# Kernel tuning notes

Measured on AMD Instinct MI355X. Metric: run time of the kernel, lower is better.

The kernel has to match this reference:

```python
import jax, jax.numpy as jnp
import numpy as np

N = 50000        # n_nodes
E = 640000       # n_edges
D = 128          # d_model (in_dim == out_dim)
H = 8            # num_heads
DH = D // H      # head dim = 16
EPS = 1e-5


def _batchnorm(x, g, b):
    # BatchNorm1d, training-mode batch statistics (biased variance)
    mu = jnp.mean(x, axis=0)
    var = jnp.mean((x - mu) ** 2, axis=0)
    return (x - mu) * jax.lax.rsqrt(var + EPS) * g + b


def setup_inputs() -> dict:
    key = jax.random.key(0)
    ks = jax.random.split(key, 16)
    s = 0.05
    h = jax.random.normal(ks[0], (N, D), jnp.float32)
    src = jax.random.randint(ks[1], (E,), 0, N)
    # guarantee every node has >= 1 incoming edge (avoids z == 0)
    dst = jnp.concatenate([jnp.arange(N), jax.random.randint(ks[2], (E - N,), 0, N)])
    return {
        "h": h,
        "src": src,
        "dst": dst,
        "WQ": jax.random.normal(ks[3], (D, D), jnp.float32) * s,
        "WK": jax.random.normal(ks[4], (D, D), jnp.float32) * s,
        "WV": jax.random.normal(ks[5], (D, D), jnp.float32) * s,
        "WO": jax.random.normal(ks[6], (D, D), jnp.float32) * s,
        "bO": jnp.zeros((D,), jnp.float32),
        "W1": jax.random.normal(ks[7], (2 * D, D), jnp.float32) * s,
        "b1": jnp.zeros((2 * D,), jnp.float32),
        "W2": jax.random.normal(ks[8], (D, 2 * D), jnp.float32) * s,
        "b2": jnp.zeros((D,), jnp.float32),
        "bn1_g": jnp.ones((D,), jnp.float32),
        "bn1_b": jnp.zeros((D,), jnp.float32),
        "bn2_g": jnp.ones((D,), jnp.float32),
        "bn2_b": jnp.zeros((D,), jnp.float32),
    }


def reference(h, src, dst, WQ, WK, WV, WO, bO, W1, b1, W2, b2, bn1_g, bn1_b, bn2_g, bn2_b):
    n = h.shape[0]
    # projections -> [N, H, DH]
    Q = (h @ WQ.T).reshape(n, H, DH)
    K = (h @ WK.T).reshape(n, H, DH)
    V = (h @ WV.T).reshape(n, H, DH)
    # per-edge score: sum(K[src] * Q[dst]) -> [E, H]; clamp/exp (scaled_exp)
    score = jnp.sum(K[src] * Q[dst], axis=-1) / np.sqrt(DH)
    score = jnp.exp(jnp.clip(score, -5.0, 5.0))
    # scatter-sum weighted values and normalizers to destination nodes
    wV = jax.ops.segment_sum(V[src] * score[..., None], dst, num_segments=n)  # [N,H,DH]
    z = jax.ops.segment_sum(score, dst, num_segments=n)                       # [N,H]
    attn = (wV / z[..., None]).reshape(n, D)
    # O projection + residual + BN1
    h1 = _batchnorm(h + (attn @ WO.T + bO), bn1_g, bn1_b)
    # FFN + residual + BN2
    f = jax.nn.relu(h1 @ W1.T + b1) @ W2.T + b2
    return _batchnorm(h1 + f, bn2_g, bn2_b)
```

## Files before the change

kernel.cpp:

```cpp
#include <hip/hip_runtime.h>
#include <math.h>


#define ND128 16384
typedef _Float16 f16;
typedef __attribute__((ext_vector_type(8))) _Float16 h8;
typedef __attribute__((ext_vector_type(4))) _Float16 h4;
typedef __attribute__((ext_vector_type(2))) _Float16 h2;
typedef __attribute__((ext_vector_type(4))) float f4;
typedef __attribute__((ext_vector_type(2))) float ff2;

__device__ __forceinline__ float fast_exp2(float x) {
#if __has_builtin(__builtin_amdgcn_exp2f)
    return __builtin_amdgcn_exp2f(x);
#else
    return exp2f(x);
#endif
}

template <int CTRL>
__device__ __forceinline__ float dppadd(float x) {
    int t = __builtin_amdgcn_update_dpp(0, __float_as_int(x), CTRL, 0xF, 0xF, false);
    return x + __int_as_float(t);
}
__device__ __forceinline__ float wsum8(float p) {
    p = dppadd<0xB1>(p);
    p = dppadd<0x4E>(p);
    p = dppadd<0x141>(p);
    return p;
}

__device__ __forceinline__ ff2 fp8x2_dec_sw(unsigned v) {
    ff2 r;
    unsigned b0 = v & 0xffu, b1 = (v >> 8) & 0xffu;
    {
        unsigned e = (b0 >> 3) & 15u, m = b0 & 7u;
        float x = e ? __uint_as_float(((e + 120u) << 23) | (m << 20)) : (float)m * 0.001953125f;
        r.x = (b0 & 0x80u) ? -x : x;
    }
    {
        unsigned e = (b1 >> 3) & 15u, m = b1 & 7u;
        float x = e ? __uint_as_float(((e + 120u) << 23) | (m << 20)) : (float)m * 0.001953125f;
        r.y = (b1 & 0x80u) ? -x : x;
    }
    return r;
}

__device__ __forceinline__ ff2 dec_lo(unsigned v) {
#if __has_builtin(__builtin_amdgcn_cvt_pk_f32_fp8)
    return __builtin_amdgcn_cvt_pk_f32_fp8((int)v, false);
#else
    return fp8x2_dec_sw(v & 0xffffu);
#endif
}
__device__ __forceinline__ ff2 dec_hi(unsigned v) {
#if __has_builtin(__builtin_amdgcn_cvt_pk_f32_fp8)
    return __builtin_amdgcn_cvt_pk_f32_fp8((int)v, true);
#else
    return fp8x2_dec_sw((v >> 16) & 0xffffu);
#endif
}

#if !__has_builtin(__builtin_amdgcn_cvt_pk_fp8_f32)
__device__ __forceinline__ unsigned char fp8_1(float f) {
    float a = fabsf(f);
    unsigned sg = (__float_as_uint(f) >> 31) << 7;
    if (a >= 448.f) return (unsigned char)(sg | 0x7E);
    if (a < 0.0009765625f) return (unsigned char)sg;
    int E; float m = frexpf(a, &E);
    if (E - 1 < -6) {
        int q = (int)rintf(a * 512.f);
        if (q > 7) return (unsigned char)(sg | 0x08);
        return (unsigned char)(sg | q);
    }
    int q = (int)rintf(m * 16.f);
    if (q == 16) { q = 8; E += 1; }
    int Ef = E - 1 + 7;
    if (Ef > 15) return (unsigned char)(sg | 0x7E);
    return (unsigned char)(sg | (Ef << 3) | (q - 8));
}
#endif

__device__ __forceinline__ unsigned short fp8_pack2(float a0, float a1) {
#if __has_builtin(__builtin_amdgcn_cvt_pk_fp8_f32)
    int pk = __builtin_amdgcn_cvt_pk_fp8_f32(a0, a1, 0, false);
    return (unsigned short)(pk & 0xffff);
#else
    return (unsigned short)((unsigned)fp8_1(a0) | ((unsigned)fp8_1(a1) << 8));
#endif
}

__global__ __launch_bounds__(256) void k_prep_hist(
    const float* __restrict__ WQ, const float* __restrict__ WK,
    const float* __restrict__ WV, const float* __restrict__ WO,
    const float* __restrict__ W2,
    f16* __restrict__ Wqb, f16* __restrict__ Wkb,
    f16* __restrict__ Wvb, f16* __restrict__ Wob, f16* __restrict__ W2b,
    int* __restrict__ cursor, const int* __restrict__ dst,
    int N, int E, int nhb)
{
    const int tid = threadIdx.x;
    if (blockIdx.x < (unsigned)nhb) {
        int e = blockIdx.x * 256 + tid;
        if (e < E) atomicAdd(&cursor[dst[e]], 1);
        return;
    }
    const int ws = blockIdx.x - nhb;
    const float* Wsrc; f16* dstw; int K, base;
    if (ws < 4) {
        Wsrc = ws == 0 ? WQ : ws == 1 ? WK : ws == 2 ? WV : WO;
        dstw = ws == 0 ? Wqb : ws == 1 ? Wkb : ws == 2 ? Wvb : Wob;
        K = 128; base = 0;
    } else {
        Wsrc = W2; dstw = W2b; K = 256; base = (ws - 4) * 2048;
    }
#pragma unroll
    for (int it = 0; it < 8; ++it) {
        int cid = base + it * 256 + tid;
        int lane = cid & 63;
        int kb, nt;
        if (K == 128) { kb = (cid >> 6) & 3; nt = cid >> 8; }
        else          { kb = (cid >> 6) & 7; nt = cid >> 9; }
        int row = nt * 16 + (lane & 15);
        int col = kb * 32 + (lane >> 4) * 8;
        const float* pp = Wsrc + (size_t)row * K + col;
        f16 o8[8];
#pragma unroll
        for (int j = 0; j < 8; ++j) o8[j] = (f16)pp[j];
        *(h8*)(dstw + (size_t)cid * 8) = *(const h8*)o8;
    }
}

__global__ __launch_bounds__(512) void k_qkvf(
    const float* __restrict__ h, f16* __restrict__ hb,
    const f16* __restrict__ Wqb, const f16* __restrict__ Wkb,
    const f16* __restrict__ Wvb,
    f16* __restrict__ Qb, unsigned char* __restrict__ KV8,
    const int* __restrict__ cursor, int* __restrict__ bsum, int N, int nsb)
{
    __shared__ f16 sA[ND128];
    __shared__ int ws8[8];
    const int tid = threadIdx.x;
    if (blockIdx.x < (unsigned)nsb) {
        int base = blockIdx.x * 2048 + tid * 4;
        int s = 0;
#pragma unroll
        for (int j = 0; j < 4; ++j) {
            int idx = base + j;
            if (idx < N) s += cursor[idx];
        }
#pragma unroll
        for (int off = 32; off; off >>= 1) s += __shfl_down(s, off, 64);
        if ((tid & 63) == 0) ws8[tid >> 6] = s;
        __syncthreads();
        if (tid == 0) {
            int r = 0;
#pragma unroll
            for (int k = 0; k < 8; ++k) r += ws8[k];
            bsum[blockIdx.x] = r;
        }
        return;
    }
    const int slab = blockIdx.x - nsb;
#pragma unroll
    for (int it = 0; it < 4; ++it) {
        int cid = it * 512 + tid;
        int lane = cid & 63;
        int m = (cid >> 6) & 7;
        int kb = cid >> 9;
        int row = slab * 128 + m * 16 + (lane & 15);
        int col = kb * 32 + (lane >> 4) * 8;
        f16 o8[8];
        if (row < N) {
            const float* pp = h + (size_t)row * 128 + col;
            float4 f0 = *(const float4*)pp;
            float4 f1 = *(const float4*)(pp + 4);
            o8[0] = (f16)f0.x; o8[1] = (f16)f0.y; o8[2] = (f16)f0.z; o8[3] = (f16)f0.w;
            o8[4] = (f16)f1.x; o8[5] = (f16)f1.y; o8[6] = (f16)f1.z; o8[7] = (f16)f1.w;
        } else {
#pragma unroll
            for (int j = 0; j < 8; ++j) o8[j] = (f16)0.f;
        }
        h8 v = *(const h8*)o8;
        *(h8*)(hb + (size_t)slab * ND128 + (size_t)cid * 8) = v;
        *(h8*)(sA + (size_t)cid * 8) = v;
    }
    __syncthreads();

    const int w2 = tid >> 6, lane = tid & 63;
    const int rl = lane & 15, quad = lane >> 4;
#pragma unroll
    for (int oidx = 0; oidx < 3; ++oidx) {
        const f16* __restrict__ Wb = oidx == 0 ? Wqb : oidx == 1 ? Wkb : Wvb;
        h8 bfr[4];
#pragma unroll
        for (int kb = 0; kb < 4; ++kb)
            bfr[kb] = *(const h8*)(Wb + (size_t)((w2 * 4 + kb) * 64 + lane) * 8);

        f4 acc[8];
        f4 zero = {0.f, 0.f, 0.f, 0.f};
#pragma unroll
        for (int m = 0; m < 8; ++m) acc[m] = zero;
#pragma unroll
        for (int m = 0; m < 8; ++m) {
#pragma unroll
            for (int kb = 0; kb < 4; ++kb) {
                h8 a = *(const h8*)(sA + (size_t)((kb * 8 + m) * 64 + lane) * 8);
                acc[m] = __builtin_amdgcn_mfma_f32_16x16x32_f16(bfr[kb], a, acc[m], 0, 0, 0);
            }
        }
        if (oidx == 0) {
#pragma unroll
            for (int m = 0; m < 8; ++m) {
                int gr = slab * 128 + m * 16 + rl;
                if (gr < N) {
                    h4 o;
                    o[0] = (f16)acc[m][0]; o[1] = (f16)acc[m][1];
                    o[2] = (f16)acc[m][2]; o[3] = (f16)acc[m][3];
                    *(h4*)(Qb + (size_t)gr * 128 + w2 * 16 + quad * 4) = o;
                }
            }
        } else {
            const int koff = (oidx == 2) ? 2 : 0;
#pragma unroll
            for (int m = 0; m < 8; ++m) {
                int gr = slab * 128 + m * 16 + rl;
                if (gr < N) {
                    int c0 = w2 * 16 + quad * 4;
                    unsigned short p01 = fp8_pack2(acc[m][0], acc[m][1]);
                    unsigned short p23 = fp8_pack2(acc[m][2], acc[m][3]);
                    unsigned char* rowp = KV8 + (size_t)gr * 256 + (size_t)c0 * 2 + koff;
                    *(unsigned short*)(rowp) = p01;
                    *(unsigned short*)(rowp + 4) = p23;
                }
            }
        }
    }
}

__global__ __launch_bounds__(256) void k_scanC(
    const int* __restrict__ cnt, const int* __restrict__ bsum,
    int* __restrict__ rowptr, int* __restrict__ cursor, int N, int nsb)
{
    const int t = threadIdx.x, b = blockIdx.x;
    __shared__ int sboff;
    if (t == 0) {
        int r = 0;
        for (int i2 = 0; i2 < b; ++i2) r += bsum[i2];
        sboff = r;
    }
    if (t == 64 && b == nsb - 1) {
        int r = 0;
        for (int i2 = 0; i2 < nsb; ++i2) r += bsum[i2];
        rowptr[N] = r;
    }
    int base = b * 2048 + t * 8;
    int loc[8];
    int s = 0;
#pragma unroll
    for (int j = 0; j < 8; ++j) {
        int idx = base + j;
        loc[j] = (idx < N) ? cnt[idx] : 0;
        s += loc[j];
    }
    __shared__ int part[256];
    part[t] = s;
    __syncthreads();
    for (int off = 1; off < 256; off <<= 1) {
        int v = (t >= off) ? part[t - off] : 0;
        __syncthreads();
        part[t] += v;
        __syncthreads();
    }
    int run = sboff + (t ? part[t - 1] : 0);
#pragma unroll
    for (int j = 0; j < 8; ++j) {
        int idx = base + j;
        if (idx < N) { rowptr[idx] = run; cursor[idx] = run; run += loc[j]; }
    }
}

__global__ __launch_bounds__(256) void k_scatter(
    const int* __restrict__ src, const int* __restrict__ dst,
    int* __restrict__ cursor, int* __restrict__ csr_src, int E)
{
    int e = blockIdx.x * 256 + threadIdx.x;
    if (e < E) {
        int pos = atomicAdd(&cursor[dst[e]], 1);
        csr_src[pos] = src[e];
    }
}

__global__ __launch_bounds__(256) void k_attn(
    const f16* __restrict__ Qb, const unsigned char* __restrict__ KV8,
    const int* __restrict__ rowptr, const int* __restrict__ csr_src,
    f16* __restrict__ attnf, int N)
{
    const int node = blockIdx.x * 4 + (threadIdx.x >> 6);
    const int lane = threadIdx.x & 63;
    if (node >= N) return;
    const int beg = rowptr[node], end = rowptr[node + 1];

    float qx, qy;
    {
        h2 q2 = ((const h2*)(Qb + (size_t)node * 128))[lane];
        const float SCL = 0.25f * 1.44269504f;
        qx = (float)q2[0] * SCL;
        qy = (float)q2[1] * SCL;
    }
    const float CLP = 5.f * 1.44269504f;
    const unsigned loff = 4u * (unsigned)lane;

    float axA = 0.f, ayA = 0.f, axB = 0.f, ayB = 0.f, zA = 0.f, zB = 0.f;
    int i = beg;
    for (; i + 7 < end; i += 8) {
        int s[8];
#pragma unroll
        for (int u = 0; u < 8; ++u) s[u] = csr_src[i + u];
        unsigned kv[8];
#pragma unroll
        for (int u = 0; u < 8; ++u)
            kv[u] = *(const unsigned*)(KV8 + (size_t)s[u] * 256 + loff);
        float p[8];
#pragma unroll
        for (int u = 0; u < 8; ++u) {
            ff2 kf = dec_lo(kv[u]);
            p[u] = fmaf(qx, kf.x, qy * kf.y);
        }
#pragma unroll
        for (int u = 0; u < 8; ++u) p[u] = wsum8(p[u]);
        float sc[8];
#pragma unroll
        for (int u = 0; u < 8; ++u)
            sc[u] = fast_exp2(fminf(fmaxf(p[u], -CLP), CLP));
#pragma unroll
        for (int u = 0; u < 8; ++u) {
            ff2 vf = dec_hi(kv[u]);
            if (u & 1) {
                axB = fmaf(vf.x, sc[u], axB); ayB = fmaf(vf.y, sc[u], ayB); zB += sc[u];
            } else {
                axA = fmaf(vf.x, sc[u], axA); ayA = fmaf(vf.y, sc[u], ayA); zA += sc[u];
            }
        }
    }
    if (i + 3 < end) {
        int s[4];
#pragma unroll
        for (int u = 0; u < 4; ++u) s[u] = csr_src[i + u];
        unsigned kv[4];
#pragma unroll
        for (int u = 0; u < 4; ++u)
            kv[u] = *(const unsigned*)(KV8 + (size_t)s[u] * 256 + loff);
#pragma unroll
        for (int u = 0; u < 4; ++u) {
            ff2 kf = dec_lo(kv[u]);
            float p = wsum8(fmaf(qx, kf.x, qy * kf.y));
            float scu = fast_exp2(fminf(fmaxf(p, -CLP), CLP));
            ff2 vf = dec_hi(kv[u]);
            if (u & 1) {
                axB = fmaf(vf.x, scu, axB); ayB = fmaf(vf.y, scu, ayB); zB += scu;
            } else {
                axA = fmaf(vf.x, scu, axA); ayA = fmaf(vf.y, scu, ayA); zA += scu;
            }
        }
        i += 4;
    }
    for (; i < end; ++i) {
        int s0 = csr_src[i];
        unsigned kv = *(const unsigned*)(KV8 + (size_t)s0 * 256 + loff);
        ff2 kf = dec_lo(kv);
        float p0 = wsum8(fmaf(qx, kf.x, qy * kf.y));
        float sc0 = fast_exp2(fminf(fmaxf(p0, -CLP), CLP));
        ff2 vf = dec_hi(kv);
        axA = fmaf(vf.x, sc0, axA); ayA = fmaf(vf.y, sc0, ayA);
        zA += sc0;
    }
    float inv = 1.f / (zA + zB);
    h2 o2;
    o2[0] = (f16)((axA + axB) * inv);
    o2[1] = (f16)((ayA + ayB) * inv);
    int slab = node >> 7, m = (node >> 4) & 7, lr = node & 15;
    int kb = lane >> 4, quad2 = (lane & 15) >> 2, j = (lane & 3) * 2;
    *(h2*)(attnf + (size_t)slab * ND128 +
           (size_t)(((kb * 8 + m) * 64 + lr + 16 * quad2) * 8 + j)) = o2;
}

__global__ __launch_bounds__(256) void k_oproj(
    const f16* __restrict__ attnf, const f16* __restrict__ Wob,
    const f16* __restrict__ hbf, const float* __restrict__ bO,
    f16* __restrict__ t1b, float* __restrict__ bn, int N)
{
    __shared__ float csum[128], csq[128];
    const int tid = threadIdx.x, slab = blockIdx.x;
    const int w = tid >> 6, lane = tid & 63;
    if (tid < 128) { csum[tid] = 0.f; csq[tid] = 0.f; }
    __syncthreads();
    const f16* A = attnf + (size_t)slab * ND128;
    const f16* HB = hbf + (size_t)slab * ND128;

    h8 bfr[2][4];
#pragma unroll
    for (int nt = 0; nt < 2; ++nt)
#pragma unroll
        for (int kb = 0; kb < 4; ++kb)
            bfr[nt][kb] = *(const h8*)(Wob + (size_t)(((2 * w + nt) * 4 + kb) * 64 + lane) * 8);

    f4 acc[8][2];
    f4 zero = {0.f, 0.f, 0.f, 0.f};
#pragma unroll
    for (int m = 0; m < 8; ++m) { acc[m][0] = zero; acc[m][1] = zero; }
#pragma unroll
    for (int m = 0; m < 8; ++m) {
#pragma unroll
        for (int kb = 0; kb < 4; ++kb) {
            h8 a = *(const h8*)(A + (size_t)((kb * 8 + m) * 64 + lane) * 8);
            acc[m][0] = __builtin_amdgcn_mfma_f32_16x16x32_f16(bfr[0][kb], a, acc[m][0], 0, 0, 0);
            acc[m][1] = __builtin_amdgcn_mfma_f32_16x16x32_f16(bfr[1][kb], a, acc[m][1], 0, 0, 0);
        }
    }

    const int rl = lane & 15, quad = lane >> 4;
    float4 bo[2];
#pragma unroll
    for (int nt = 0; nt < 2; ++nt)
        bo[nt] = *(const float4*)(bO + w * 32 + nt * 16 + quad * 4);
    float pcs[2][4], pcq[2][4];
#pragma unroll
    for (int nt = 0; nt < 2; ++nt)
#pragma unroll
        for (int r = 0; r < 4; ++r) { pcs[nt][r] = 0.f; pcq[nt][r] = 0.f; }

#pragma unroll
    for (int m = 0; m < 8; ++m) {
        int gr = slab * 128 + m * 16 + rl;
        if (gr < N) {
#pragma unroll
            for (int nt = 0; nt < 2; ++nt) {
                size_t fidx = (size_t)(((w * 8 + m) * 64 + (nt * 2 + (quad >> 1)) * 16 + rl) * 8 +
                                       (quad & 1) * 4);
                h4 hv4 = *(const h4*)(HB + fidx);
                float v0 = acc[m][nt][0] + (float)hv4[0] + bo[nt].x;
                float v1 = acc[m][nt][1] + (float)hv4[1] + bo[nt].y;
                float v2 = acc[m][nt][2] + (float)hv4[2] + bo[nt].z;
                float v3 = acc[m][nt][3] + (float)hv4[3] + bo[nt].w;
                h4 o; o[0] = (f16)v0; o[1] = (f16)v1; o[2] = (f16)v2; o[3] = (f16)v3;
                *(h4*)(t1b + (size_t)slab * ND128 + fidx) = o;
                pcs[nt][0] += v0; pcq[nt][0] += v0 * v0;
                pcs[nt][1] += v1; pcq[nt][1] += v1 * v1;
                pcs[nt][2] += v2; pcq[nt][2] += v2 * v2;
                pcs[nt][3] += v3; pcq[nt][3] += v3 * v3;
            }
        }
    }
#pragma unroll
    for (int nt = 0; nt < 2; ++nt)
#pragma unroll
        for (int r = 0; r < 4; ++r) {
            float s = pcs[nt][r], q = pcq[nt][r];
            s += __shfl_xor(s, 8, 16); q += __shfl_xor(q, 8, 16);
            s += __shfl_xor(s, 4, 16); q += __shfl_xor(q, 4, 16);
            s += __shfl_xor(s, 2, 16); q += __shfl_xor(q, 2, 16);
            s += __shfl_xor(s, 1, 16); q += __shfl_xor(q, 1, 16);
            if (rl == 0) {
                int cl = w * 32 + nt * 16 + quad * 4 + r;
                atomicAdd(&csum[cl], s);
                atomicAdd(&csq[cl], q);
            }
        }
    __syncthreads();
    if (tid < 128) {
        atomicAdd(bn + tid, csum[tid]);
        atomicAdd(bn + 128 + tid, csq[tid]);
    }
}

__global__ __launch_bounds__(128) void k_fold1(
    const float* __restrict__ bn, const float* __restrict__ g1,
    const float* __restrict__ bb1, const float* __restrict__ W1,
    const float* __restrict__ b1, f16* __restrict__ W1b,
    float* __restrict__ badj, float* __restrict__ sfold,
    float* __restrict__ bfold, int N)
{
    const int o = blockIdx.x, i = threadIdx.x;
    float invN = 1.f / (float)N;
    float mu = bn[i] * invN;
    float var = bn[128 + i] * invN - mu * mu;
    float s = g1[i] * rsqrtf(var + 1e-5f);
    float bb = bb1[i] - mu * s;
    if (o == 0) { sfold[i] = s; bfold[i] = bb; }
    float wv = W1[(size_t)o * 128 + i];
    __shared__ float red[128];
    red[i] = wv * bb;
    const int nt = o >> 4, lanelow = o & 15;
    const int kb = i >> 5, quad = (i >> 3) & 3, j = i & 7;
    W1b[(size_t)(((nt * 4 + kb) * 64 + lanelow + 16 * quad) * 8 + j)] = (f16)(wv * s);
    __syncthreads();
#pragma unroll
    for (int off = 64; off; off >>= 1) {
        if (i < off) red[i] += red[i + off];
        __syncthreads();
    }
    if (i == 0) badj[o] = b1[o] + red[0];
}

__global__ __launch_bounds__(512) void k_ffn(
    const f16* __restrict__ t1b, const f16* __restrict__ W1b,
    const float* __restrict__ badj, const f16* __restrict__ W2b,
    const float* __restrict__ sfold, const float* __restrict__ bfold,
    const float* __restrict__ b2, f16* __restrict__ t2f,
    float* __restrict__ bn, int N)
{
    __shared__ f16 uf[32768];
    const int tid = threadIdx.x, slab = blockIdx.x;
    const int w2 = tid >> 6, lane = tid & 63;
    const int rl = lane & 15, quad = lane >> 4;
    const f16* T1 = t1b + (size_t)slab * ND128;

    {
        h8 bfr[2][4];
#pragma unroll
        for (int nt = 0; nt < 2; ++nt) {
            int ntg = w2 * 2 + nt;
#pragma unroll
            for (int kb = 0; kb < 4; ++kb)
                bfr[nt][kb] = *(const h8*)(W1b + (size_t)((ntg * 4 + kb) * 64 + lane) * 8);
        }
        f4 acc[8][2];
        f4 zero = {0.f, 0.f, 0.f, 0.f};
#pragma unroll
        for (int m = 0; m < 8; ++m) { acc[m][0] = zero; acc[m][1] = zero; }
#pragma unroll
        for (int m = 0; m < 8; ++m) {
#pragma unroll
            for (int kb = 0; kb < 4; ++kb) {
                h8 a = *(const h8*)(T1 + (size_t)((kb * 8 + m) * 64 + lane) * 8);
                acc[m][0] = __builtin_amdgcn_mfma_f32_16x16x32_f16(bfr[0][kb], a, acc[m][0], 0, 0, 0);
                acc[m][1] = __builtin_amdgcn_mfma_f32_16x16x32_f16(bfr[1][kb], a, acc[m][1], 0, 0, 0);
            }
        }
        float4 ba[2];
#pragma unroll
        for (int nt = 0; nt < 2; ++nt)
            ba[nt] = *(const float4*)(badj + (w2 * 2 + nt) * 16 + quad * 4);
#pragma unroll
        for (int m = 0; m < 8; ++m) {
#pragma unroll
            for (int nt = 0; nt < 2; ++nt) {
                h4 o;
                o[0] = (f16)fmaxf(acc[m][nt][0] + ba[nt].x, 0.f);
                o[1] = (f16)fmaxf(acc[m][nt][1] + ba[nt].y, 0.f);
                o[2] = (f16)fmaxf(acc[m][nt][2] + ba[nt].z, 0.f);
                o[3] = (f16)fmaxf(acc[m][nt][3] + ba[nt].w, 0.f);
                *(h4*)(uf + (size_t)(((w2 * 8 + m) * 64 +
                       (nt * 2 + (quad >> 1)) * 16 + rl) * 8 + (quad & 1) * 4)) = o;
            }
        }
    }
    __syncthreads();

    {
        h8 bfr2[8];
#pragma unroll
        for (int kb = 0; kb < 8; ++kb)
            bfr2[kb] = *(const h8*)(W2b + (size_t)((w2 * 8 + kb) * 64 + lane) * 8);

        f4 acc2[8];
        f4 zero = {0.f, 0.f, 0.f, 0.f};
#pragma unroll
        for (int m = 0; m < 8; ++m) acc2[m] = zero;
#pragma unroll
        for (int m = 0; m < 8; ++m) {
#pragma unroll
            for (int kb = 0; kb < 8; ++kb) {
                h8 a = *(const h8*)(uf + (size_t)((kb * 8 + m) * 64 + lane) * 8);
                acc2[m] = __builtin_amdgcn_mfma_f32_16x16x32_f16(bfr2[kb], a, acc2[m], 0, 0, 0);
            }
        }

        const int c0 = w2 * 16 + quad * 4;
        float4 ss = *(const float4*)(sfold + c0);
        float4 sbA = *(const float4*)(bfold + c0);
        float4 sbB = *(const float4*)(b2 + c0);
        float4 sb;
        sb.x = sbA.x + sbB.x; sb.y = sbA.y + sbB.y;
        sb.z = sbA.z + sbB.z; sb.w = sbA.w + sbB.w;

        float pcs[4] = {0.f, 0.f, 0.f, 0.f};
        float pcq[4] = {0.f, 0.f, 0.f, 0.f};
#pragma unroll
        for (int m = 0; m < 8; ++m) {
            int gr = slab * 128 + m * 16 + rl;
            if (gr < N) {
                size_t fidx = (size_t)((((w2 >> 1) * 8 + m) * 64 +
                              ((w2 & 1) * 2 + (quad >> 1)) * 16 + rl) * 8 + (quad & 1) * 4);
                h4 t1v = *(const h4*)(T1 + fidx);
                h4 o2;
                o2[0] = (f16)(acc2[m][0] + fmaf(ss.x, (float)t1v[0], sb.x));
                o2[1] = (f16)(acc2[m][1] + fmaf(ss.y, (float)t1v[1], sb.y));
                o2[2] = (f16)(acc2[m][2] + fmaf(ss.z, (float)t1v[2], sb.z));
                o2[3] = (f16)(acc2[m][3] + fmaf(ss.w, (float)t1v[3], sb.w));
                *(h4*)(t2f + (size_t)slab * ND128 + fidx) = o2;
                float r0 = (float)o2[0], r1 = (float)o2[1];
                float r2 = (float)o2[2], r3 = (float)o2[3];
                pcs[0] += r0; pcq[0] += r0 * r0;
                pcs[1] += r1; pcq[1] += r1 * r1;
                pcs[2] += r2; pcq[2] += r2 * r2;
                pcs[3] += r3; pcq[3] += r3 * r3;
            }
        }
#pragma unroll
        for (int r = 0; r < 4; ++r) {
            float s = pcs[r], q = pcq[r];
            s += __shfl_xor(s, 8, 16); q += __shfl_xor(q, 8, 16);
            s += __shfl_xor(s, 4, 16); q += __shfl_xor(q, 4, 16);
            s += __shfl_xor(s, 2, 16); q += __shfl_xor(q, 2, 16);
            s += __shfl_xor(s, 1, 16); q += __shfl_xor(q, 1, 16);
            if (rl == 0) {
                int cl = c0 + r;
                atomicAdd(bn + 256 + cl, s);
                atomicAdd(bn + 384 + cl, q);
            }
        }
    }
}

__global__ __launch_bounds__(256) void k_bn2(
    const f16* __restrict__ t2f, float* __restrict__ out,
    const float* __restrict__ bn,
    const float* __restrict__ g2, const float* __restrict__ bb2, int N)
{
    __shared__ float sS[128], sB[128];
    const int tid = threadIdx.x;
    if (tid < 128) {
        float invN = 1.f / (float)N;
        float mu = bn[256 + tid] * invN;
        float var = bn[384 + tid] * invN - mu * mu;
        float scl = g2[tid] * rsqrtf(var + 1e-5f);
        sS[tid] = scl;
        sB[tid] = bb2[tid] - mu * scl;
    }
    __syncthreads();
    size_t idx = (size_t)blockIdx.x * 256 + tid;
    size_t total = (size_t)N * 32;
    if (idx < total) {
        int gr = (int)(idx >> 5);
        int c0 = ((int)idx & 31) * 4;
        int slab = gr >> 7, m = (gr >> 4) & 7, rl = gr & 15;
        int w = c0 >> 5, nt = (c0 >> 4) & 1, q = (c0 >> 2) & 3;
        size_t fidx = (size_t)(((w * 8 + m) * 64 + (nt * 2 + (q >> 1)) * 16 + rl) * 8 +
                               (q & 1) * 4);
        h4 v = *(const h4*)(t2f + (size_t)slab * ND128 + fidx);
        float4 o;
        o.x = fmaf((float)v[0], sS[c0 + 0], sB[c0 + 0]);
        o.y = fmaf((float)v[1], sS[c0 + 1], sB[c0 + 1]);
        o.z = fmaf((float)v[2], sS[c0 + 2], sB[c0 + 2]);
        o.w = fmaf((float)v[3], sS[c0 + 3], sB[c0 + 3]);
        *(float4*)(out + (size_t)gr * 128 + c0) = o;
    }
}

extern "C" void kernel_launch(void* const* d_in, const int* in_sizes, int n_in,
                              void* d_out, int out_size, void* d_ws, size_t ws_size,
                              hipStream_t stream)
{
    const float* h   = (const float*)d_in[0];
    const int*   src = (const int*)d_in[1];
    const int*   dst = (const int*)d_in[2];
    const float* WQ  = (const float*)d_in[3];
    const float* WK  = (const float*)d_in[4];
    const float* WV  = (const float*)d_in[5];
    const float* WO  = (const float*)d_in[6];
    const float* bO  = (const float*)d_in[7];
    const float* W1  = (const float*)d_in[8];
    const float* b1  = (const float*)d_in[9];
    const float* W2  = (const float*)d_in[10];
    const float* b2  = (const float*)d_in[11];
    const float* g1  = (const float*)d_in[12];
    const float* bb1 = (const float*)d_in[13];
    const float* g2  = (const float*)d_in[14];
    const float* bb2 = (const float*)d_in[15];
    float* out = (float*)d_out;

    int N = in_sizes[0] / 128;
    int E = in_sizes[1];
    int slabs = (N + 127) / 128;
    int nsb = (N + 2047) / 2048;
    int nhb = (E + 255) / 256;
    const size_t B1 = (size_t)slabs * 32768;

    char* Wp = (char*)d_ws;
    f16* hb  = (f16*)Wp;
    f16* Qb  = (f16*)(Wp + B1);
    unsigned char* KV8 = (unsigned char*)(Wp + 2 * B1);
    f16* attnf = (f16*)(Wp + 3 * B1);
    f16* t1b = (f16*)(Wp + 4 * B1);
    f16* t2f = attnf;
    const size_t base = 5 * B1;
    f16* Wqb = (f16*)(Wp + base);
    f16* Wkb = (f16*)(Wp + base + 32768);
    f16* Wvb = (f16*)(Wp + base + 65536);
    f16* Wob = (f16*)(Wp + base + 98304);
    f16* W1b = (f16*)(Wp + base + 131072);
    f16* W2b = (f16*)(Wp + base + 196608);
    float* badj  = (float*)(Wp + base + 262144);
    float* sfold = (float*)(Wp + base + 263168);
    float* bfold = (float*)(Wp + base + 263680);
    float* bn    = (float*)(Wp + base + 264192);
    int* bsum    = (int*)(Wp + base + 266240);
    int* cursor  = (int*)(Wp + base + 266496);
    int* rowptr  = (int*)(Wp + base + 266496 + (size_t)N * 4);
    int* csr     = (int*)(Wp + base + 266496 + (size_t)N * 8 + 8);

    hipMemsetAsync(Wp + base + 264192, 0, 2304 + (size_t)N * 4, stream);
    k_prep_hist<<<nhb + 6, 256, 0, stream>>>(
        WQ, WK, WV, WO, W2, Wqb, Wkb, Wvb, Wob, W2b, cursor, dst, N, E, nhb);
    k_qkvf<<<nsb + slabs, 512, 0, stream>>>(
        h, hb, Wqb, Wkb, Wvb, Qb, KV8, cursor, bsum, N, nsb);
    k_scanC<<<nsb, 256, 0, stream>>>(cursor, bsum, rowptr, cursor, N, nsb);
    k_scatter<<<nhb, 256, 0, stream>>>(src, dst, cursor, csr, E);
    k_attn<<<(N + 3) / 4, 256, 0, stream>>>(Qb, KV8, rowptr, csr, attnf, N);
    k_oproj<<<slabs, 256, 0, stream>>>(attnf, Wob, hb, bO, t1b, bn, N);
    k_fold1<<<256, 128, 0, stream>>>(bn, g1, bb1, W1, b1, W1b, badj, sfold, bfold, N);
    k_ffn<<<slabs, 512, 0, stream>>>(t1b, W1b, badj, W2b, sfold, bfold, b2, t2f, bn, N);
    k_bn2<<<(int)(((size_t)N * 32 + 255) / 256), 256, 0, stream>>>(t2f, out, bn, g2, bb2, N);
}
```

Measured before the change: 313.1 us.

## Split FFN into two kernels via global buffer and widen O-projection blocks

The fused FFN kernel, which kept the 256-wide hidden activation in 64KB of shared memory, is split into k_ffn1 (GEMM1 + ReLU written to a global fp16 buffer reusing the Q workspace) and k_ffn2 (GEMM2 + residual + BN2 stats). The aim is to drop the large LDS footprint and its barrier so more blocks can be resident per CU. k_oproj moves to 512 threads with one 16-column tile per wave, halving per-wave accumulators, and k_ffn2 now reduces BN stats through shared memory before the global atomics. The cost is an extra launch and a global round trip for the hidden activation (about 25MB written and read).

```diff
diff --git a/kernel.cpp b/kernel.cpp
--- a/kernel.cpp
+++ b/kernel.cpp
@@ -385,88 +385,73 @@
            (size_t)(((kb * 8 + m) * 64 + lr + 16 * quad2) * 8 + j)) = o2;
 }
 
-__global__ __launch_bounds__(256) void k_oproj(
+__global__ __launch_bounds__(512) void k_oproj(
     const f16* __restrict__ attnf, const f16* __restrict__ Wob,
     const f16* __restrict__ hbf, const float* __restrict__ bO,
     f16* __restrict__ t1b, float* __restrict__ bn, int N)
 {
     __shared__ float csum[128], csq[128];
     const int tid = threadIdx.x, slab = blockIdx.x;
-    const int w = tid >> 6, lane = tid & 63;
+    const int w2 = tid >> 6, lane = tid & 63;
+    const int rl = lane & 15, quad = lane >> 4;
     if (tid < 128) { csum[tid] = 0.f; csq[tid] = 0.f; }
     __syncthreads();
     const f16* A = attnf + (size_t)slab * ND128;
     const f16* HB = hbf + (size_t)slab * ND128;
 
-    h8 bfr[2][4];
-#pragma unroll
-    for (int nt = 0; nt < 2; ++nt)
-#pragma unroll
-        for (int kb = 0; kb < 4; ++kb)
-            bfr[nt][kb] = *(const h8*)(Wob + (size_t)(((2 * w + nt) * 4 + kb) * 64 + lane) * 8);
-
-    f4 acc[8][2];
+    h8 bfr[4];
+#pragma unroll
+    for (int kb = 0; kb < 4; ++kb)
+        bfr[kb] = *(const h8*)(Wob + (size_t)((w2 * 4 + kb) * 64 + lane) * 8);
+
+    f4 acc[8];
     f4 zero = {0.f, 0.f, 0.f, 0.f};
 #pragma unroll
-    for (int m = 0; m < 8; ++m) { acc[m][0] = zero; acc[m][1] = zero; }
+    for (int m = 0; m < 8; ++m) acc[m] = zero;
 #pragma unroll
     for (int m = 0; m < 8; ++m) {
 #pragma unroll
         for (int kb = 0; kb < 4; ++kb) {
             h8 a = *(const h8*)(A + (size_t)((kb * 8 + m) * 64 + lane) * 8);
-            acc[m][0] = __builtin_amdgcn_mfma_f32_16x16x32_f16(bfr[0][kb], a, acc[m][0], 0, 0, 0);
-            acc[m][1] = __builtin_amdgcn_mfma_f32_16x16x32_f16(bfr[1][kb], a, acc[m][1], 0, 0, 0);
-        }
-    }
-
-    const int rl = lane & 15, quad = lane >> 4;
-    float4 bo[2];
-#pragma unroll
-    for (int nt = 0; nt < 2; ++nt)
-        bo[nt] = *(const float4*)(bO + w * 32 + nt * 16 + quad * 4);
-    float pcs[2][4], pcq[2][4];
-#pragma unroll
-    for (int nt = 0; nt < 2; ++nt)
-#pragma unroll
-        for (int r = 0; r < 4; ++r) { pcs[nt][r] = 0.f; pcq[nt][r] = 0.f; }
-
+            acc[m] = __builtin_amdgcn_mfma_f32_16x16x32_f16(bfr[kb], a, acc[m], 0, 0, 0);
+        }
+    }
+
+    const int c0 = w2 * 16 + quad * 4;
+    float4 bo = *(const float4*)(bO + c0);
+    float pcs[4] = {0.f, 0.f, 0.f, 0.f};
+    float pcq[4] = {0.f, 0.f, 0.f, 0.f};
 #pragma unroll
     for (int m = 0; m < 8; ++m) {
         int gr = slab * 128 + m * 16 + rl;
         if (gr < N) {
-#pragma unroll
-            for (int nt = 0; nt < 2; ++nt) {
-                size_t fidx = (size_t)(((w * 8 + m) * 64 + (nt * 2 + (quad >> 1)) * 16 + rl) * 8 +
-                                       (quad & 1) * 4);
-                h4 hv4 = *(const h4*)(HB + fidx);
-                float v0 = acc[m][nt][0] + (float)hv4[0] + bo[nt].x;
-                float v1 = acc[m][nt][1] + (float)hv4[1] + bo[nt].y;
-                float v2 = acc[m][nt][2] + (float)hv4[2] + bo[nt].z;
-                float v3 = acc[m][nt][3] + (float)hv4[3] + bo[nt].w;
-                h4 o; o[0] = (f16)v0; o[1] = (f16)v1; o[2] = (f16)v2; o[3] = (f16)v3;
-                *(h4*)(t1b + (size_t)slab * ND128 + fidx) = o;
-                pcs[nt][0] += v0; pcq[nt][0] += v0 * v0;
-                pcs[nt][1] += v1; pcq[nt][1] += v1 * v1;
-                pcs[nt][2] += v2; pcq[nt][2] += v2 * v2;
-                pcs[nt][3] += v3; pcq[nt][3] += v3 * v3;
-            }
-        }
-    }
-#pragma unroll
-    for (int nt = 0; nt < 2; ++nt)
-#pragma unroll
-        for (int r = 0; r < 4; ++r) {
-            float s = pcs[nt][r], q = pcq[nt][r];
-            s += __shfl_xor(s, 8, 16); q += __shfl_xor(q, 8, 16);
-            s += __shfl_xor(s, 4, 16); q += __shfl_xor(q, 4, 16);
-            s += __shfl_xor(s, 2, 16); q += __shfl_xor(q, 2, 16);
-            s += __shfl_xor(s, 1, 16); q += __shfl_xor(q, 1, 16);
-            if (rl == 0) {
-                int cl = w * 32 + nt * 16 + quad * 4 + r;
-                atomicAdd(&csum[cl], s);
-                atomicAdd(&csq[cl], q);
-            }
-        }
+            size_t fidx = (size_t)((((w2 >> 1) * 8 + m) * 64 +
+                          ((w2 & 1) * 2 + (quad >> 1)) * 16 + rl) * 8 + (quad & 1) * 4);
+            h4 hv4 = *(const h4*)(HB + fidx);
+            float v0 = acc[m][0] + (float)hv4[0] + bo.x;
+            float v1 = acc[m][1] + (float)hv4[1] + bo.y;
+            float v2 = acc[m][2] + (float)hv4[2] + bo.z;
+            float v3 = acc[m][3] + (float)hv4[3] + bo.w;
+            h4 o; o[0] = (f16)v0; o[1] = (f16)v1; o[2] = (f16)v2; o[3] = (f16)v3;
+            *(h4*)(t1b + (size_t)slab * ND128 + fidx) = o;
+            pcs[0] += v0; pcq[0] += v0 * v0;
+            pcs[1] += v1; pcq[1] += v1 * v1;
+            pcs[2] += v2; pcq[2] += v2 * v2;
+            pcs[3] += v3; pcq[3] += v3 * v3;
+        }
+    }
+#pragma unroll
+    for (int r = 0; r < 4; ++r) {
+        float s = pcs[r], q = pcq[r];
+        s += __shfl_xor(s, 8, 16); q += __shfl_xor(q, 8, 16);
+        s += __shfl_xor(s, 4, 16); q += __shfl_xor(q, 4, 16);
+        s += __shfl_xor(s, 2, 16); q += __shfl_xor(q, 2, 16);
+        s += __shfl_xor(s, 1, 16); q += __shfl_xor(q, 1, 16);
+        if (rl == 0) {
+            atomicAdd(&csum[c0 + r], s);
+            atomicAdd(&csq[c0 + r], q);
+        }
+    }
     __syncthreads();
     if (tid < 128) {
         atomicAdd(bn + tid, csum[tid]);
@@ -503,47 +488,48 @@
     if (i == 0) badj[o] = b1[o] + red[0];
 }
 
-__global__ __launch_bounds__(512) void k_ffn(
+__global__ __launch_bounds__(512) void k_ffn1(
     const f16* __restrict__ t1b, const f16* __restrict__ W1b,
-    const float* __restrict__ badj, const f16* __restrict__ W2b,
-    const float* __restrict__ sfold, const float* __restrict__ bfold,
-    const float* __restrict__ b2, f16* __restrict__ t2f,
-    float* __restrict__ bn, int N)
-{
-    __shared__ f16 uf[32768];
-    const int tid = threadIdx.x, slab = blockIdx.x;
-    const int w2 = tid >> 6, lane = tid & 63;
+    const float* __restrict__ badj, f16* __restrict__ ub, int N)
+{
+    const int slab = blockIdx.x;
+    const int w2 = threadIdx.x >> 6, lane = threadIdx.x & 63;
+    const int ch = w2 >> 2, wl = w2 & 3;
+    const f16* A = t1b + (size_t)slab * ND128;
+
+    h8 bfr[2][4];
+#pragma unroll
+    for (int nt = 0; nt < 2; ++nt)
+#pragma unroll
+        for (int kb = 0; kb < 4; ++kb) {
+            int ntg = ch * 8 + 2 * wl + nt;
+            bfr[nt][kb] = *(const h8*)(W1b + (size_t)((ntg * 4 + kb) * 64 + lane) * 8);
+        }
+
+    f4 acc[8][2];
+    f4 zero = {0.f, 0.f, 0.f, 0.f};
+#pragma unroll
+    for (int m = 0; m < 8; ++m) { acc[m][0] = zero; acc[m][1] = zero; }
+#pragma unroll
+    for (int m = 0; m < 8; ++m) {
+#pragma unroll
+        for (int kb = 0; kb < 4; ++kb) {
+            h8 a = *(const h8*)(A + (size_t)((kb * 8 + m) * 64 + lane) * 8);
+            acc[m][0] = __builtin_amdgcn_mfma_f32_16x16x32_f16(bfr[0][kb], a, acc[m][0], 0, 0, 0);
+            acc[m][1] = __builtin_amdgcn_mfma_f32_16x16x32_f16(bfr[1][kb], a, acc[m][1], 0, 0, 0);
+        }
+    }
+
     const int rl = lane & 15, quad = lane >> 4;
-    const f16* T1 = t1b + (size_t)slab * ND128;
-
-    {
-        h8 bfr[2][4];
-#pragma unroll
-        for (int nt = 0; nt < 2; ++nt) {
-            int ntg = w2 * 2 + nt;
-#pragma unroll
-            for (int kb = 0; kb < 4; ++kb)
-                bfr[nt][kb] = *(const h8*)(W1b + (size_t)((ntg * 4 + kb) * 64 + lane) * 8);
-        }
-        f4 acc[8][2];
-        f4 zero = {0.f, 0.f, 0.f, 0.f};
-#pragma unroll
-        for (int m = 0; m < 8; ++m) { acc[m][0] = zero; acc[m][1] = zero; }
-#pragma unroll
-        for (int m = 0; m < 8; ++m) {
-#pragma unroll
-            for (int kb = 0; kb < 4; ++kb) {
-                h8 a = *(const h8*)(T1 + (size_t)((kb * 8 + m) * 64 + lane) * 8);
-                acc[m][0] = __builtin_amdgcn_mfma_f32_16x16x32_f16(bfr[0][kb], a, acc[m][0], 0, 0, 0);
-                acc[m][1] = __builtin_amdgcn_mfma_f32_16x16x32_f16(bfr[1][kb], a, acc[m][1], 0, 0, 0);
-            }
-        }
-        float4 ba[2];
-#pragma unroll
-        for (int nt = 0; nt < 2; ++nt)
-            ba[nt] = *(const float4*)(badj + (w2 * 2 + nt) * 16 + quad * 4);
-#pragma unroll
-        for (int m = 0; m < 8; ++m) {
+    const int kbu = ch * 4 + wl;
+    float4 ba[2];
+#pragma unroll
+    for (int nt = 0; nt < 2; ++nt)
+        ba[nt] = *(const float4*)(badj + ch * 128 + wl * 32 + nt * 16 + quad * 4);
+#pragma unroll
+    for (int m = 0; m < 8; ++m) {
+        int gr = slab * 128 + m * 16 + rl;
+        if (gr < N) {
 #pragma unroll
             for (int nt = 0; nt < 2; ++nt) {
                 h4 o;
@@ -551,76 +537,95 @@
                 o[1] = (f16)fmaxf(acc[m][nt][1] + ba[nt].y, 0.f);
                 o[2] = (f16)fmaxf(acc[m][nt][2] + ba[nt].z, 0.f);
                 o[3] = (f16)fmaxf(acc[m][nt][3] + ba[nt].w, 0.f);
-                *(h4*)(uf + (size_t)(((w2 * 8 + m) * 64 +
-                       (nt * 2 + (quad >> 1)) * 16 + rl) * 8 + (quad & 1) * 4)) = o;
+                *(h4*)(ub + (size_t)slab * 32768 +
+                       (size_t)(((kbu * 8 + m) * 64 + (nt * 2 + (quad >> 1)) * 16 + rl) * 8 +
+                                (quad & 1) * 4)) = o;
             }
         }
     }
+}
+
+__global__ __launch_bounds__(512) void k_ffn2(
+    const f16* __restrict__ ub, const f16* __restrict__ W2b,
+    const f16* __restrict__ t1b,
+    const float* __restrict__ sfold, const float* __restrict__ bfold,
+    const float* __restrict__ b2, f16* __restrict__ t2f,
+    float* __restrict__ bn, int N)
+{
+    __shared__ float csum[128], csq[128];
+    const int tid = threadIdx.x, slab = blockIdx.x;
+    const int w2 = tid >> 6, lane = tid & 63;
+    const int rl = lane & 15, quad = lane >> 4;
+    if (tid < 128) { csum[tid] = 0.f; csq[tid] = 0.f; }
     __syncthreads();
-
-    {
-        h8 bfr2[8];
-#pragma unroll
-        for (int kb = 0; kb < 8; ++kb)
-            bfr2[kb] = *(const h8*)(W2b + (size_t)((w2 * 8 + kb) * 64 + lane) * 8);
-
-        f4 acc2[8];
-        f4 zero = {0.f, 0.f, 0.f, 0.f};
-#pragma unroll
-        for (int m = 0; m < 8; ++m) acc2[m] = zero;
-#pragma unroll
-        for (int m = 0; m < 8; ++m) {
-#pragma unroll
-            for (int kb = 0; kb < 8; ++kb) {
-                h8 a = *(const h8*)(uf + (size_t)((kb * 8 + m) * 64 + lane) * 8);
-                acc2[m] = __builtin_amdgcn_mfma_f32_16x16x32_f16(bfr2[kb], a, acc2[m], 0, 0, 0);
-            }
-        }
-
-        const int c0 = w2 * 16 + quad * 4;
-        float4 ss = *(const float4*)(sfold + c0);
-        float4 sbA = *(const float4*)(bfold + c0);
-        float4 sbB = *(const float4*)(b2 + c0);
-        float4 sb;
-        sb.x = sbA.x + sbB.x; sb.y = sbA.y + sbB.y;
-        sb.z = sbA.z + sbB.z; sb.w = sbA.w + sbB.w;
-
-        float pcs[4] = {0.f, 0.f, 0.f, 0.f};
-        float pcq[4] = {0.f, 0.f, 0.f, 0.f};
-#pragma unroll
-        for (int m = 0; m < 8; ++m) {
-            int gr = slab * 128 + m * 16 + rl;
-            if (gr < N) {
-                size_t fidx = (size_t)((((w2 >> 1) * 8 + m) * 64 +
-                              ((w2 & 1) * 2 + (quad >> 1)) * 16 + rl) * 8 + (quad & 1) * 4);
-                h4 t1v = *(const h4*)(T1 + fidx);
-                h4 o2;
-                o2[0] = (f16)(acc2[m][0] + fmaf(ss.x, (float)t1v[0], sb.x));
-                o2[1] = (f16)(acc2[m][1] + fmaf(ss.y, (float)t1v[1], sb.y));
-                o2[2] = (f16)(acc2[m][2] + fmaf(ss.z, (float)t1v[2], sb.z));
-                o2[3] = (f16)(acc2[m][3] + fmaf(ss.w, (float)t1v[3], sb.w));
-                *(h4*)(t2f + (size_t)slab * ND128 + fidx) = o2;
-                float r0 = (float)o2[0], r1 = (float)o2[1];
-                float r2 = (float)o2[2], r3 = (float)o2[3];
-                pcs[0] += r0; pcq[0] += r0 * r0;
-                pcs[1] += r1; pcq[1] += r1 * r1;
-                pcs[2] += r2; pcq[2] += r2 * r2;
-                pcs[3] += r3; pcq[3] += r3 * r3;
-            }
-        }
-#pragma unroll
-        for (int r = 0; r < 4; ++r) {
-            float s = pcs[r], q = pcq[r];
-            s += __shfl_xor(s, 8, 16); q += __shfl_xor(q, 8, 16);
-            s += __shfl_xor(s, 4, 16); q += __shfl_xor(q, 4, 16);
-            s += __shfl_xor(s, 2, 16); q += __shfl_xor(q, 2, 16);
-            s += __shfl_xor(s, 1, 16); q += __shfl_xor(q, 1, 16);
-            if (rl == 0) {
-                int cl = c0 + r;
-                atomicAdd(bn + 256 + cl, s);
-                atomicAdd(bn + 384 + cl, q);
-            }
-        }
+    const f16* A = ub + (size_t)slab * 32768;
+    const f16* T1 = t1b + (size_t)slab * ND128;
+
+    h8 bfr2[8];
+#pragma unroll
+    for (int kb = 0; kb < 8; ++kb)
+        bfr2[kb] = *(const h8*)(W2b + (size_t)((w2 * 8 + kb) * 64 + lane) * 8);
+
+    f4 acc2[8];
+    f4 zero = {0.f, 0.f, 0.f, 0.f};
+#pragma unroll
+    for (int m = 0; m < 8; ++m) acc2[m] = zero;
+#pragma unroll
+    for (int m = 0; m < 8; ++m) {
+#pragma unroll
+        for (int kb = 0; kb < 8; ++kb) {
+            h8 a = *(const h8*)(A + (size_t)((kb * 8 + m) * 64 + lane) * 8);
+            acc2[m] = __builtin_amdgcn_mfma_f32_16x16x32_f16(bfr2[kb], a, acc2[m], 0, 0, 0);
+        }
+    }
+
+    const int c0 = w2 * 16 + quad * 4;
+    float4 ss = *(const float4*)(sfold + c0);
+    float4 sbA = *(const float4*)(bfold + c0);
+    float4 sbB = *(const float4*)(b2 + c0);
+    float4 sb;
+    sb.x = sbA.x + sbB.x; sb.y = sbA.y + sbB.y;
+    sb.z = sbA.z + sbB.z; sb.w = sbA.w + sbB.w;
+
+    float pcs[4] = {0.f, 0.f, 0.f, 0.f};
+    float pcq[4] = {0.f, 0.f, 0.f, 0.f};
+#pragma unroll
+    for (int m = 0; m < 8; ++m) {
+        int gr = slab * 128 + m * 16 + rl;
+        if (gr < N) {
+            size_t fidx = (size_t)((((w2 >> 1) * 8 + m) * 64 +
+                          ((w2 & 1) * 2 + (quad >> 1)) * 16 + rl) * 8 + (quad & 1) * 4);
+            h4 t1v = *(const h4*)(T1 + fidx);
+            h4 o2;
+            o2[0] = (f16)(acc2[m][0] + fmaf(ss.x, (float)t1v[0], sb.x));
+            o2[1] = (f16)(acc2[m][1] + fmaf(ss.y, (float)t1v[1], sb.y));
+            o2[2] = (f16)(acc2[m][2] + fmaf(ss.z, (float)t1v[2], sb.z));
+            o2[3] = (f16)(acc2[m][3] + fmaf(ss.w, (float)t1v[3], sb.w));
+            *(h4*)(t2f + (size_t)slab * ND128 + fidx) = o2;
+            float r0 = (float)o2[0], r1 = (float)o2[1];
+            float r2 = (float)o2[2], r3 = (float)o2[3];
+            pcs[0] += r0; pcq[0] += r0 * r0;
+            pcs[1] += r1; pcq[1] += r1 * r1;
+            pcs[2] += r2; pcq[2] += r2 * r2;
+            pcs[3] += r3; pcq[3] += r3 * r3;
+        }
+    }
+#pragma unroll
+    for (int r = 0; r < 4; ++r) {
+        float s = pcs[r], q = pcq[r];
+        s += __shfl_xor(s, 8, 16); q += __shfl_xor(q, 8, 16);
+        s += __shfl_xor(s, 4, 16); q += __shfl_xor(q, 4, 16);
+        s += __shfl_xor(s, 2, 16); q += __shfl_xor(q, 2, 16);
+        s += __shfl_xor(s, 1, 16); q += __shfl_xor(q, 1, 16);
+        if (rl == 0) {
+            atomicAdd(&csum[c0 + r], s);
+            atomicAdd(&csq[c0 + r], q);
+        }
+    }
+    __syncthreads();
+    if (tid < 128) {
+        atomicAdd(bn + 256 + tid, csum[tid]);
+        atomicAdd(bn + 384 + tid, csq[tid]);
     }
 }
 
@@ -694,6 +699,7 @@
     unsigned char* KV8 = (unsigned char*)(Wp + 2 * B1);
     f16* attnf = (f16*)(Wp + 3 * B1);
     f16* t1b = (f16*)(Wp + 4 * B1);
+    f16* ub  = (f16*)(Wp + B1);
     f16* t2f = attnf;
     const size_t base = 5 * B1;
     f16* Wqb = (f16*)(Wp + base);
@@ -719,8 +725,9 @@
     k_scanC<<<nsb, 256, 0, stream>>>(cursor, bsum, rowptr, cursor, N, nsb);
     k_scatter<<<nhb, 256, 0, stream>>>(src, dst, cursor, csr, E);
     k_attn<<<(N + 3) / 4, 256, 0, stream>>>(Qb, KV8, rowptr, csr, attnf, N);
-    k_oproj<<<slabs, 256, 0, stream>>>(attnf, Wob, hb, bO, t1b, bn, N);
+    k_oproj<<<slabs, 512, 0, stream>>>(attnf, Wob, hb, bO, t1b, bn, N);
     k_fold1<<<256, 128, 0, stream>>>(bn, g1, bb1, W1, b1, W1b, badj, sfold, bfold, N);
-    k_ffn<<<slabs, 512, 0, stream>>>(t1b, W1b, badj, W2b, sfold, bfold, b2, t2f, bn, N);
+    k_ffn1<<<slabs, 512, 0, stream>>>(t1b, W1b, badj, ub, N);
+    k_ffn2<<<slabs, 512, 0, stream>>>(ub, W2b, t1b, sfold, bfold, b2, t2f, bn, N);
     k_bn2<<<(int)(((size_t)N * 32 + 255) / 256), 256, 0, stream>>>(t2f, out, bn, g2, bb2, N);
 }
```

Measured after the change: 288.6 us. 7.8% less time.
